# Performance work log

Hardware: AMD Instinct MI355X
Metric: run time of the kernel (lower is better)

## Reference

```python
import jax, jax.numpy as jnp
import numpy as np

N4, N3, N2, N1, K = 32768, 65536, 131072, 262144, 16
G = 512


def _w(key, fan_in, fan_out):
    return jax.random.normal(key, (fan_in, fan_out), dtype=jnp.float32) / np.sqrt(fan_in)


def setup_inputs() -> dict:
    key = jax.random.key(0)
    ks = jax.random.split(key, 24)

    def edges(k, n_coarse, n_fine):
        # each fine (output) point gathers from K random coarse (input) points
        src = jax.random.randint(k, (n_fine * K,), 0, n_coarse, dtype=jnp.int32)
        dst = jnp.repeat(jnp.arange(n_fine, dtype=jnp.int32), K)
        return src, dst

    src3, dst3 = edges(ks[0], N4, N3)
    src2, dst2 = edges(ks[1], N3, N2)
    src1, dst1 = edges(ks[2], N2, N1)

    def gidx(k, n):
        return jnp.sort(jax.random.randint(k, (n,), 0, G, dtype=jnp.int32))

    inp = {
        'z_mask': jax.random.normal(ks[3], (N4, 64), dtype=jnp.float32),
        'pos4': jax.random.normal(ks[4], (N4, 3), dtype=jnp.float32),
        'pos3': jax.random.normal(ks[5], (N3, 3), dtype=jnp.float32),
        'pos2': jax.random.normal(ks[6], (N2, 3), dtype=jnp.float32),
        'pos1': jax.random.normal(ks[7], (N1, 3), dtype=jnp.float32),
        'g4': gidx(ks[8], N4), 'g3': gidx(ks[9], N3),
        'g2': gidx(ks[10], N2), 'g1': gidx(ks[11], N1),
        # PointConv MLP params: Linear(c_in+3 -> c_mid), CELU, Linear(c_mid -> c_out), max-aggregate
        'w1a': _w(ks[12], 64 + 3, 64), 'b1a': jnp.zeros((64,), jnp.float32),
        'w1b': _w(ks[13], 64, 32), 'b1b': jnp.zeros((32,), jnp.float32),
        'w2a': _w(ks[14], 32 + 3, 16), 'b2a': jnp.zeros((16,), jnp.float32),
        'w2b': _w(ks[15], 16, 16), 'b2b': jnp.zeros((16,), jnp.float32),
        'w3a': _w(ks[16], 16 + 3, 8), 'b3a': jnp.zeros((8,), jnp.float32),
        'w3b': _w(ks[17], 8, 8), 'b3b': jnp.zeros((8,), jnp.float32),
        'wlin': _w(ks[18], 8, 1), 'blin': jnp.zeros((1,), jnp.float32),
        'src3': src3, 'dst3': dst3,
        'src2': src2, 'dst2': dst2,
        'src1': src1, 'dst1': dst1,
    }
    return inp


def point_conv(x_in, pos_in, pos_out, src, dst, w_a, b_a, w_b, b_b, n_out):
    # gather: per-edge neighbor features + relative positions
    rel = pos_in[src] - pos_out[dst]                      # [E, 3]
    feat = jnp.concatenate([x_in[src], rel], axis=-1)     # [E, c_in+3]
    h = jax.nn.celu(feat @ w_a + b_a)                     # [E, c_mid]
    m = h @ w_b + b_b                                     # [E, c_out]
    # scatter: max-aggregate edge messages onto output points
    return jax.ops.segment_max(m, dst, num_segments=n_out)


def reference(z_mask, pos4, pos3, pos2, pos1, g4, g3, g2, g1,
              w1a, b1a, w1b, b1b, w2a, b2a, w2b, b2b, w3a, b3a, w3b, b3b,
              wlin, blin, src3, dst3, src2, dst2, src1, dst1):
    out = jax.nn.celu(point_conv(z_mask, pos4, pos3, src3, dst3, w1a, b1a, w1b, b1b, N3))
    out = jax.nn.celu(point_conv(out, pos3, pos2, src2, dst2, w2a, b2a, w2b, b2b, N2))
    out = jax.nn.celu(point_conv(out, pos2, pos1, src1, dst1, w3a, b3a, w3b, b3b, N1))
    logits = out @ wlin + blin                            # [N1, 1]
    return jax.nn.log_sigmoid(logits)
```

## Files before the change

### kernel.cpp

```cpp
#include <hip/hip_runtime.h>
#include <hip/hip_fp16.h>
#include <math.h>

#define N4C 32768
#define N3C 65536
#define N2C 131072
#define N1C 262144

typedef _Float16 f16x8 __attribute__((ext_vector_type(8)));
typedef float f32x4 __attribute__((ext_vector_type(4)));
typedef float f32x16 __attribute__((ext_vector_type(16)));

__device__ __forceinline__ f32x4 mfma16(f16x8 a, f16x8 b, f32x4 c) {
  return __builtin_amdgcn_mfma_f32_16x16x32_f16(a, b, c, 0, 0, 0);
}
__device__ __forceinline__ f32x16 mfma32(f16x8 a, f16x8 b, f32x16 c) {
  return __builtin_amdgcn_mfma_f32_32x32x16_f16(a, b, c, 0, 0, 0);
}

__device__ __forceinline__ float celuf(float x) {
  return fmaxf(x, 0.f) + (__expf(fminf(x, 0.f)) - 1.f);
}

__device__ __forceinline__ float logsigf(float x) {
  float e = __expf(-fabsf(x));
  return fminf(x, 0.f) - __logf(1.f + e);
}

__device__ __forceinline__ _Float16 exp16(_Float16 x) {
  __half h; __builtin_memcpy(&h, &x, 2);
  h = hexp(h);
  _Float16 r; __builtin_memcpy(&r, &h, 2);
  return r;
}

__device__ __forceinline__ f16x8 celu8(f16x8 x) {
  f16x8 z = {};
  f16x8 mx = __builtin_elementwise_max(x, z);
  f16x8 mn = __builtin_elementwise_min(x, z);
#pragma unroll
  for (int i = 0; i < 8; ++i) mn[i] = exp16(mn[i]);
  return mx + (mn - (_Float16)1.0f);
}

__device__ __forceinline__ unsigned packh2(_Float16 a, _Float16 b) {
  union { _Float16 h[2]; unsigned u; } v; v.h[0] = a; v.h[1] = b; return v.u;
}
__device__ __forceinline__ _Float16 loh(unsigned u) {
  union { unsigned u; _Float16 h[2]; } v; v.u = u; return v.h[0];
}
__device__ __forceinline__ _Float16 hih(unsigned u) {
  union { unsigned u; _Float16 h[2]; } v; v.u = u; return v.h[1];
}

__global__ __launch_bounds__(256) void y4_kernel(
    const float* __restrict__ z, const float* __restrict__ w1a,
    const float* __restrict__ b1a, _Float16* __restrict__ y4) {
  const int lane = threadIdx.x & 63, wid = threadIdx.x >> 6;
  const int col = lane & 15, quad = lane >> 4;
  const int base = (blockIdx.x * 4 + wid) * 16;

  f16x8 Ba[2][4];
#pragma unroll
  for (int c = 0; c < 2; ++c)
#pragma unroll
    for (int t = 0; t < 4; ++t)
#pragma unroll
      for (int j = 0; j < 8; ++j)
        Ba[c][t][j] = (_Float16)w1a[(c * 32 + quad * 8 + j) * 64 + t * 16 + col];

  const float* zr = z + (size_t)(base + col) * 64;
  f16x8 A0, A1;
  {
    float4 f0 = *(const float4*)(zr + quad * 8);
    float4 f1 = *(const float4*)(zr + quad * 8 + 4);
    float4 f2 = *(const float4*)(zr + 32 + quad * 8);
    float4 f3 = *(const float4*)(zr + 32 + quad * 8 + 4);
    A0[0] = (_Float16)f0.x; A0[1] = (_Float16)f0.y; A0[2] = (_Float16)f0.z; A0[3] = (_Float16)f0.w;
    A0[4] = (_Float16)f1.x; A0[5] = (_Float16)f1.y; A0[6] = (_Float16)f1.z; A0[7] = (_Float16)f1.w;
    A1[0] = (_Float16)f2.x; A1[1] = (_Float16)f2.y; A1[2] = (_Float16)f2.z; A1[3] = (_Float16)f2.w;
    A1[4] = (_Float16)f3.x; A1[5] = (_Float16)f3.y; A1[6] = (_Float16)f3.z; A1[7] = (_Float16)f3.w;
  }
#pragma unroll
  for (int t = 0; t < 4; ++t) {
    f32x4 acc = {0.f, 0.f, 0.f, 0.f};
    acc = mfma16(A0, Ba[0][t], acc);
    acc = mfma16(A1, Ba[1][t], acc);
    const float bt = b1a[t * 16 + col];
#pragma unroll
    for (int r = 0; r < 4; ++r)
      y4[(size_t)(base + quad * 4 + r) * 64 + t * 16 + col] = (_Float16)(acc[r] + bt);
  }
}

__global__ __launch_bounds__(256) void y3_kernel(
    const _Float16* __restrict__ x3f, const float* __restrict__ w2a,
    const float* __restrict__ b2a, _Float16* __restrict__ y3) {
  const int lane = threadIdx.x & 63, wid = threadIdx.x >> 6;
  const int col = lane & 15, quad = lane >> 4;
  const int base = (blockIdx.x * 4 + wid) * 16;

  f16x8 B;
#pragma unroll
  for (int j = 0; j < 8; ++j) B[j] = (_Float16)w2a[(quad * 8 + j) * 16 + col];

  f16x8 A = *(const f16x8*)(x3f + (size_t)(base + col) * 32 + quad * 8);
  f32x4 d = {0.f, 0.f, 0.f, 0.f};
  d = mfma16(A, B, d);
  const float bt = b2a[col];
#pragma unroll
  for (int r = 0; r < 4; ++r)
    y3[(size_t)(base + quad * 4 + r) * 16 + col] = (_Float16)(d[r] + bt);
}

__global__ __launch_bounds__(256) void y2_kernel(
    const _Float16* __restrict__ x2f, const float* __restrict__ w3a,
    const float* __restrict__ b3a, _Float16* __restrict__ y2) {
  const int lane = threadIdx.x & 63, wid = threadIdx.x >> 6;
  const int col = lane & 15, quad = lane >> 4;
  const int base = (blockIdx.x * 4 + wid) * 16;

  f16x8 B;
#pragma unroll
  for (int j = 0; j < 8; ++j) {
    int k = quad * 8 + j;
    B[j] = (k < 16 && col < 8) ? (_Float16)w3a[k * 8 + col] : (_Float16)0.f;
  }
  f16x8 A = *(const f16x8*)(x2f + (size_t)(base + col) * 16 + (quad & 1) * 8);
  f32x4 d = {0.f, 0.f, 0.f, 0.f};
  d = mfma16(A, B, d);
  if (col < 8) {
    const float bt = b3a[col];
#pragma unroll
    for (int r = 0; r < 4; ++r)
      y2[(size_t)(base + quad * 4 + r) * 8 + col] = (_Float16)(d[r] + bt);
  }
}

__global__ __launch_bounds__(256) void l3_kernel(
    const _Float16* __restrict__ y4, const float* __restrict__ pos4,
    const float* __restrict__ pos3, const int* __restrict__ src3,
    const float* __restrict__ w1a, const float* __restrict__ w1b,
    const float* __restrict__ b1b, _Float16* __restrict__ x3f) {
  const int lane = threadIdx.x & 63, wid = threadIdx.x >> 6;
  const int col = lane & 15, quad = lane >> 4;

  f16x8 Bb[2][2];
#pragma unroll
  for (int c = 0; c < 2; ++c)
#pragma unroll
    for (int t = 0; t < 2; ++t)
#pragma unroll
      for (int j = 0; j < 8; ++j)
        Bb[c][t][j] = (_Float16)w1b[(c * 32 + quad * 8 + j) * 32 + t * 16 + col];
  f16x8 W0[3], W1[3];
#pragma unroll
  for (int c = 0; c < 3; ++c)
#pragma unroll
    for (int j = 0; j < 8; ++j) {
      W0[c][j] = (_Float16)w1a[(64 + c) * 64 + quad * 8 + j];
      W1[c][j] = (_Float16)w1a[(64 + c) * 64 + 32 + quad * 8 + j];
    }
  const float biasB0 = b1b[col], biasB1 = b1b[16 + col];

  const int gwave = blockIdx.x * 4 + wid;
  const int nw = gridDim.x * 4;

  for (int p = gwave; p < N3C; p += nw) {
    const int s = src3[p * 16 + col];
    const int up = __builtin_amdgcn_readfirstlane(p);
    const float po0 = pos3[up * 3 + 0];
    const float po1 = pos3[up * 3 + 1];
    const float po2 = pos3[up * 3 + 2];

    f16x8 A0 = *(const f16x8*)(y4 + (size_t)s * 64 + quad * 8);
    f16x8 A1 = *(const f16x8*)(y4 + (size_t)s * 64 + 32 + quad * 8);

    unsigned u0 = 0, u1 = 0;
    if (quad == 0) {
      _Float16 h0 = (_Float16)(pos4[s * 3 + 0] - po0);
      _Float16 h1 = (_Float16)(pos4[s * 3 + 1] - po1);
      _Float16 h2 = (_Float16)(pos4[s * 3 + 2] - po2);
      u0 = packh2(h0, h1);
      u1 = packh2(h2, (_Float16)0.f);
    }
    u0 = (unsigned)__shfl((int)u0, col, 64);
    u1 = (unsigned)__shfl((int)u1, col, 64);
    const _Float16 rr0 = loh(u0), rr1 = hih(u0), rr2 = loh(u1);

    A0 = celu8(A0 + W0[0] * rr0 + W0[1] * rr1 + W0[2] * rr2);
    A1 = celu8(A1 + W1[0] * rr0 + W1[1] * rr1 + W1[2] * rr2);

    f32x4 e[2];
#pragma unroll
    for (int t = 0; t < 2; ++t) {
      f32x4 acc = {0.f, 0.f, 0.f, 0.f};
      acc = mfma16(A0, Bb[0][t], acc);
      acc = mfma16(A1, Bb[1][t], acc);
      e[t] = acc;
    }
    float m0 = fmaxf(fmaxf(e[0][0], e[0][1]), fmaxf(e[0][2], e[0][3]));
    float m1 = fmaxf(fmaxf(e[1][0], e[1][1]), fmaxf(e[1][2], e[1][3]));
    m0 = fmaxf(m0, __shfl_xor(m0, 16, 64));
    m0 = fmaxf(m0, __shfl_xor(m0, 32, 64));
    m1 = fmaxf(m1, __shfl_xor(m1, 16, 64));
    m1 = fmaxf(m1, __shfl_xor(m1, 32, 64));
    if (lane < 16) {
      _Float16* row = x3f + (size_t)p * 32;
      row[col]      = (_Float16)celuf(m0 + biasB0);
      row[16 + col] = (_Float16)celuf(m1 + biasB1);
    }
  }
}

__global__ __launch_bounds__(256) void l2_kernel(
    const _Float16* __restrict__ y3, const float* __restrict__ pos3,
    const float* __restrict__ pos2, const int* __restrict__ src2,
    const float* __restrict__ w2a, const float* __restrict__ w2b,
    const float* __restrict__ b2b, _Float16* __restrict__ x2f) {
  const int lane = threadIdx.x & 63, wid = threadIdx.x >> 6;
  const int n = lane & 31;
  const int e = lane & 15;
  const int h = (lane >> 4) & 1;
  const int kh = lane >> 5;

  f16x8 Bb;
#pragma unroll
  for (int j = 0; j < 8; ++j)
    Bb[j] = (n < 16) ? (_Float16)w2b[(kh * 8 + j) * 16 + n] : (_Float16)0.f;
  f16x8 W[3];
#pragma unroll
  for (int c = 0; c < 3; ++c)
#pragma unroll
    for (int j = 0; j < 8; ++j)
      W[c][j] = (_Float16)w2a[(32 + c) * 16 + kh * 8 + j];
  const float biasB = b2b[n & 15];

  const int gwave = blockIdx.x * 4 + wid;
  const int nw = gridDim.x * 4;

  for (int pr = gwave; pr < N2C / 2; pr += nw) {
    const int p = 2 * pr + h;
    const int s = src2[p * 16 + e];

    f16x8 A = *(const f16x8*)(y3 + (size_t)s * 16 + kh * 8);

    unsigned u0 = 0, u1 = 0;
    if (kh == 0) {
      _Float16 h0 = (_Float16)(pos3[s * 3 + 0] - pos2[p * 3 + 0]);
      _Float16 h1 = (_Float16)(pos3[s * 3 + 1] - pos2[p * 3 + 1]);
      _Float16 h2 = (_Float16)(pos3[s * 3 + 2] - pos2[p * 3 + 2]);
      u0 = packh2(h0, h1);
      u1 = packh2(h2, (_Float16)0.f);
    }
    u0 = (unsigned)__shfl((int)u0, lane & 31, 64);
    u1 = (unsigned)__shfl((int)u1, lane & 31, 64);
    const _Float16 rr0 = loh(u0), rr1 = hih(u0), rr2 = loh(u1);

    A = celu8(A + W[0] * rr0 + W[1] * rr1 + W[2] * rr2);

    f32x16 acc = {};
    acc = mfma32(A, Bb, acc);

    float mA = acc[0], mB = acc[8];
#pragma unroll
    for (int r = 1; r < 8; ++r) {
      mA = fmaxf(mA, acc[r]);
      mB = fmaxf(mB, acc[8 + r]);
    }
    mA = fmaxf(mA, __shfl_xor(mA, 32, 64));
    mB = fmaxf(mB, __shfl_xor(mB, 32, 64));

    if (n < 16) {
      const float m = kh ? mB : mA;
      x2f[(size_t)(2 * pr + kh) * 16 + n] = (_Float16)celuf(m + biasB);
    }
  }
}

__global__ __launch_bounds__(256) void l1_kernel(
    const _Float16* __restrict__ y2, const float* __restrict__ pos2,
    const float* __restrict__ pos1, const int* __restrict__ src1,
    const float* __restrict__ w3a, const float* __restrict__ w3b,
    const float* __restrict__ b3b, const float* __restrict__ wlin,
    const float* __restrict__ blin, float* __restrict__ out) {
  const int lane = threadIdx.x & 63, wid = threadIdx.x >> 6;
  const int m = lane & 31;
  const int e = lane & 15;
  const int h = (lane >> 4) & 1;
  const int kh = lane >> 5;
  const int g = 2 * kh + h;

  f16x8 Bb;
  const int n = m;
#pragma unroll
  for (int j = 0; j < 8; ++j)
    Bb[j] = (n < 16 && (n >> 3) == kh) ? (_Float16)w3b[j * 8 + (n & 7)]
                                       : (_Float16)0.f;
  f16x8 W[3];
#pragma unroll
  for (int c = 0; c < 3; ++c)
#pragma unroll
    for (int j = 0; j < 8; ++j)
      W[c][j] = (_Float16)w3a[(16 + c) * 8 + j];
  const float biasB = (n < 16) ? b3b[n & 7] : 0.f;
  const float wl = (n < 16) ? wlin[n & 7] : 0.f;
  const float bl = blin[0];

  const int gwave = blockIdx.x * 4 + wid;
  const int nw = gridDim.x * 4;

  for (int q = gwave; q < N1C / 4; q += nw) {
    const int pb = q * 4;
    const int p = pb + g;
    const int s = src1[p * 16 + e];

    f16x8 A = *(const f16x8*)(y2 + (size_t)s * 8);
    const _Float16 rr0 = (_Float16)(pos2[s * 3 + 0] - pos1[p * 3 + 0]);
    const _Float16 rr1 = (_Float16)(pos2[s * 3 + 1] - pos1[p * 3 + 1]);
    const _Float16 rr2 = (_Float16)(pos2[s * 3 + 2] - pos1[p * 3 + 2]);
    A = celu8(A + W[0] * rr0 + W[1] * rr1 + W[2] * rr2);

    f32x16 acc = {};
    acc = mfma32(A, Bb, acc);

    float mA = acc[0], mB = acc[8];
#pragma unroll
    for (int r = 1; r < 8; ++r) {
      mA = fmaxf(mA, acc[r]);
      mB = fmaxf(mB, acc[8 + r]);
    }
    mA = fmaxf(mA, __shfl_xor(mA, 32, 64));
    mB = fmaxf(mB, __shfl_xor(mB, 32, 64));
    float tA = celuf(mA + biasB) * wl;
    float tB = celuf(mB + biasB) * wl;
    tA += __shfl_xor(tA, 1, 64);
    tA += __shfl_xor(tA, 2, 64);
    tA += __shfl_xor(tA, 4, 64);
    tB += __shfl_xor(tB, 1, 64);
    tB += __shfl_xor(tB, 2, 64);
    tB += __shfl_xor(tB, 4, 64);
    if (lane == 0) {
      float2 o; o.x = logsigf(tA + bl); o.y = logsigf(tB + bl);
      *(float2*)(out + pb) = o;
    } else if (lane == 8) {
      float2 o; o.x = logsigf(tA + bl); o.y = logsigf(tB + bl);
      *(float2*)(out + pb + 2) = o;
    }
  }
}

extern "C" void kernel_launch(void* const* d_in, const int* in_sizes, int n_in,
                              void* d_out, int out_size, void* d_ws, size_t ws_size,
                              hipStream_t stream) {
  const float* z_mask = (const float*)d_in[0];
  const float* pos4 = (const float*)d_in[1];
  const float* pos3 = (const float*)d_in[2];
  const float* pos2 = (const float*)d_in[3];
  const float* pos1 = (const float*)d_in[4];
  const float* w1a = (const float*)d_in[9];
  const float* b1a = (const float*)d_in[10];
  const float* w1b = (const float*)d_in[11];
  const float* b1b = (const float*)d_in[12];
  const float* w2a = (const float*)d_in[13];
  const float* b2a = (const float*)d_in[14];
  const float* w2b = (const float*)d_in[15];
  const float* b2b = (const float*)d_in[16];
  const float* w3a = (const float*)d_in[17];
  const float* b3a = (const float*)d_in[18];
  const float* w3b = (const float*)d_in[19];
  const float* b3b = (const float*)d_in[20];
  const float* wlin = (const float*)d_in[21];
  const float* blin = (const float*)d_in[22];
  const int* src3 = (const int*)d_in[23];
  const int* src2 = (const int*)d_in[25];
  const int* src1 = (const int*)d_in[27];

  char* w = (char*)d_ws;
  _Float16* y4  = (_Float16*)(w);
  _Float16* x3f = (_Float16*)(w + (4u << 20));
  _Float16* y3  = (_Float16*)(w + (8u << 20));
  _Float16* x2f = (_Float16*)(w + (10u << 20));
  _Float16* y2  = (_Float16*)(w + (14u << 20));
  float* out = (float*)d_out;

  y4_kernel<<<512, 256, 0, stream>>>(z_mask, w1a, b1a, y4);
  l3_kernel<<<2048, 256, 0, stream>>>(y4, pos4, pos3, src3, w1a, w1b, b1b, x3f);
  y3_kernel<<<1024, 256, 0, stream>>>(x3f, w2a, b2a, y3);
  l2_kernel<<<8192, 256, 0, stream>>>(y3, pos3, pos2, src2, w2a, w2b, b2b, x2f);
  y2_kernel<<<2048, 256, 0, stream>>>(x2f, w3a, b3a, y2);
  l1_kernel<<<8192, 256, 0, stream>>>(y2, pos2, pos1, src1, w3a, w3b, b3b,
                                      wlin, blin, out);
}
```

Before: 262.6 us.

## Fold source-position term into per-point precomputed projections to drop per-edge pos gathers

```diff
diff --git a/kernel.cpp b/kernel.cpp
--- a/kernel.cpp
+++ b/kernel.cpp
@@ -43,19 +43,10 @@
   return mx + (mn - (_Float16)1.0f);
 }
 
-__device__ __forceinline__ unsigned packh2(_Float16 a, _Float16 b) {
-  union { _Float16 h[2]; unsigned u; } v; v.h[0] = a; v.h[1] = b; return v.u;
-}
-__device__ __forceinline__ _Float16 loh(unsigned u) {
-  union { unsigned u; _Float16 h[2]; } v; v.u = u; return v.h[0];
-}
-__device__ __forceinline__ _Float16 hih(unsigned u) {
-  union { unsigned u; _Float16 h[2]; } v; v.u = u; return v.h[1];
-}
-
 __global__ __launch_bounds__(256) void y4_kernel(
-    const float* __restrict__ z, const float* __restrict__ w1a,
-    const float* __restrict__ b1a, _Float16* __restrict__ y4) {
+    const float* __restrict__ z, const float* __restrict__ pos4,
+    const float* __restrict__ w1a, const float* __restrict__ b1a,
+    _Float16* __restrict__ y4) {
   const int lane = threadIdx.x & 63, wid = threadIdx.x >> 6;
   const int col = lane & 15, quad = lane >> 4;
   const int base = (blockIdx.x * 4 + wid) * 16;
@@ -68,6 +59,22 @@
 #pragma unroll
       for (int j = 0; j < 8; ++j)
         Ba[c][t][j] = (_Float16)w1a[(c * 32 + quad * 8 + j) * 64 + t * 16 + col];
+
+  float wr[3][4];
+#pragma unroll
+  for (int c = 0; c < 3; ++c)
+#pragma unroll
+    for (int t = 0; t < 4; ++t)
+      wr[c][t] = w1a[(64 + c) * 64 + t * 16 + col];
+
+  float px[4], py[4], pz[4];
+#pragma unroll
+  for (int r = 0; r < 4; ++r) {
+    const int row = base + quad * 4 + r;
+    px[r] = pos4[row * 3 + 0];
+    py[r] = pos4[row * 3 + 1];
+    pz[r] = pos4[row * 3 + 2];
+  }
 
   const float* zr = z + (size_t)(base + col) * 64;
   f16x8 A0, A1;
@@ -88,14 +95,19 @@
     acc = mfma16(A1, Ba[1][t], acc);
     const float bt = b1a[t * 16 + col];
 #pragma unroll
-    for (int r = 0; r < 4; ++r)
-      y4[(size_t)(base + quad * 4 + r) * 64 + t * 16 + col] = (_Float16)(acc[r] + bt);
+    for (int r = 0; r < 4; ++r) {
+      const float posterm =
+          px[r] * wr[0][t] + py[r] * wr[1][t] + pz[r] * wr[2][t];
+      y4[(size_t)(base + quad * 4 + r) * 64 + t * 16 + col] =
+          (_Float16)(acc[r] + bt + posterm);
+    }
   }
 }
 
 __global__ __launch_bounds__(256) void y3_kernel(
-    const _Float16* __restrict__ x3f, const float* __restrict__ w2a,
-    const float* __restrict__ b2a, _Float16* __restrict__ y3) {
+    const _Float16* __restrict__ x3f, const float* __restrict__ pos3,
+    const float* __restrict__ w2a, const float* __restrict__ b2a,
+    _Float16* __restrict__ y3) {
   const int lane = threadIdx.x & 63, wid = threadIdx.x >> 6;
   const int col = lane & 15, quad = lane >> 4;
   const int base = (blockIdx.x * 4 + wid) * 16;
@@ -103,19 +115,36 @@
   f16x8 B;
 #pragma unroll
   for (int j = 0; j < 8; ++j) B[j] = (_Float16)w2a[(quad * 8 + j) * 16 + col];
+
+  float wr[3];
+#pragma unroll
+  for (int c = 0; c < 3; ++c) wr[c] = w2a[(32 + c) * 16 + col];
+
+  float px[4], py[4], pz[4];
+#pragma unroll
+  for (int r = 0; r < 4; ++r) {
+    const int row = base + quad * 4 + r;
+    px[r] = pos3[row * 3 + 0];
+    py[r] = pos3[row * 3 + 1];
+    pz[r] = pos3[row * 3 + 2];
+  }
 
   f16x8 A = *(const f16x8*)(x3f + (size_t)(base + col) * 32 + quad * 8);
   f32x4 d = {0.f, 0.f, 0.f, 0.f};
   d = mfma16(A, B, d);
   const float bt = b2a[col];
 #pragma unroll
-  for (int r = 0; r < 4; ++r)
-    y3[(size_t)(base + quad * 4 + r) * 16 + col] = (_Float16)(d[r] + bt);
+  for (int r = 0; r < 4; ++r) {
+    const float posterm = px[r] * wr[0] + py[r] * wr[1] + pz[r] * wr[2];
+    y3[(size_t)(base + quad * 4 + r) * 16 + col] =
+        (_Float16)(d[r] + bt + posterm);
+  }
 }
 
 __global__ __launch_bounds__(256) void y2_kernel(
-    const _Float16* __restrict__ x2f, const float* __restrict__ w3a,
-    const float* __restrict__ b3a, _Float16* __restrict__ y2) {
+    const _Float16* __restrict__ x2f, const float* __restrict__ pos2,
+    const float* __restrict__ w3a, const float* __restrict__ b3a,
+    _Float16* __restrict__ y2) {
   const int lane = threadIdx.x & 63, wid = threadIdx.x >> 6;
   const int col = lane & 15, quad = lane >> 4;
   const int base = (blockIdx.x * 4 + wid) * 16;
@@ -130,18 +159,26 @@
   f32x4 d = {0.f, 0.f, 0.f, 0.f};
   d = mfma16(A, B, d);
   if (col < 8) {
+    float wr[3];
+#pragma unroll
+    for (int c = 0; c < 3; ++c) wr[c] = w3a[(16 + c) * 8 + col];
     const float bt = b3a[col];
 #pragma unroll
-    for (int r = 0; r < 4; ++r)
-      y2[(size_t)(base + quad * 4 + r) * 8 + col] = (_Float16)(d[r] + bt);
+    for (int r = 0; r < 4; ++r) {
+      const int row = base + quad * 4 + r;
+      const float posterm = pos2[row * 3 + 0] * wr[0] +
+                            pos2[row * 3 + 1] * wr[1] +
+                            pos2[row * 3 + 2] * wr[2];
+      y2[(size_t)row * 8 + col] = (_Float16)(d[r] + bt + posterm);
+    }
   }
 }
 
 __global__ __launch_bounds__(256) void l3_kernel(
-    const _Float16* __restrict__ y4, const float* __restrict__ pos4,
-    const float* __restrict__ pos3, const int* __restrict__ src3,
-    const float* __restrict__ w1a, const float* __restrict__ w1b,
-    const float* __restrict__ b1b, _Float16* __restrict__ x3f) {
+    const _Float16* __restrict__ y4, const float* __restrict__ pos3,
+    const int* __restrict__ src3, const float* __restrict__ w1a,
+    const float* __restrict__ w1b, const float* __restrict__ b1b,
+    _Float16* __restrict__ x3f) {
   const int lane = threadIdx.x & 63, wid = threadIdx.x >> 6;
   const int col = lane & 15, quad = lane >> 4;
 
@@ -169,27 +206,18 @@
   for (int p = gwave; p < N3C; p += nw) {
     const int s = src3[p * 16 + col];
     const int up = __builtin_amdgcn_readfirstlane(p);
-    const float po0 = pos3[up * 3 + 0];
-    const float po1 = pos3[up * 3 + 1];
-    const float po2 = pos3[up * 3 + 2];
+    const _Float16 q0 = (_Float16)pos3[up * 3 + 0];
+    const _Float16 q1 = (_Float16)pos3[up * 3 + 1];
+    const _Float16 q2 = (_Float16)pos3[up * 3 + 2];
 
     f16x8 A0 = *(const f16x8*)(y4 + (size_t)s * 64 + quad * 8);
     f16x8 A1 = *(const f16x8*)(y4 + (size_t)s * 64 + 32 + quad * 8);
 
-    unsigned u0 = 0, u1 = 0;
-    if (quad == 0) {
-      _Float16 h0 = (_Float16)(pos4[s * 3 + 0] - po0);
-      _Float16 h1 = (_Float16)(pos4[s * 3 + 1] - po1);
-      _Float16 h2 = (_Float16)(pos4[s * 3 + 2] - po2);
-      u0 = packh2(h0, h1);
-      u1 = packh2(h2, (_Float16)0.f);
-    }
-    u0 = (unsigned)__shfl((int)u0, col, 64);
-    u1 = (unsigned)__shfl((int)u1, col, 64);
-    const _Float16 rr0 = loh(u0), rr1 = hih(u0), rr2 = loh(u1);
-
-    A0 = celu8(A0 + W0[0] * rr0 + W0[1] * rr1 + W0[2] * rr2);
-    A1 = celu8(A1 + W1[0] * rr0 + W1[1] * rr1 + W1[2] * rr2);
+    const f16x8 v0 = W0[0] * q0 + W0[1] * q1 + W0[2] * q2;
+    const f16x8 v1 = W1[0] * q0 + W1[1] * q1 + W1[2] * q2;
+
+    A0 = celu8(A0 - v0);
+    A1 = celu8(A1 - v1);
 
     f32x4 e[2];
 #pragma unroll
@@ -214,10 +242,10 @@
 }
 
 __global__ __launch_bounds__(256) void l2_kernel(
-    const _Float16* __restrict__ y3, const float* __restrict__ pos3,
-    const float* __restrict__ pos2, const int* __restrict__ src2,
-    const float* __restrict__ w2a, const float* __restrict__ w2b,
-    const float* __restrict__ b2b, _Float16* __restrict__ x2f) {
+    const _Float16* __restrict__ y3, const float* __restrict__ pos2,
+    const int* __restrict__ src2, const float* __restrict__ w2a,
+    const float* __restrict__ w2b, const float* __restrict__ b2b,
+    _Float16* __restrict__ x2f) {
   const int lane = threadIdx.x & 63, wid = threadIdx.x >> 6;
   const int n = lane & 31;
   const int e = lane & 15;
@@ -243,21 +271,13 @@
     const int p = 2 * pr + h;
     const int s = src2[p * 16 + e];
 
+    const _Float16 q0 = (_Float16)pos2[p * 3 + 0];
+    const _Float16 q1 = (_Float16)pos2[p * 3 + 1];
+    const _Float16 q2 = (_Float16)pos2[p * 3 + 2];
+
     f16x8 A = *(const f16x8*)(y3 + (size_t)s * 16 + kh * 8);
-
-    unsigned u0 = 0, u1 = 0;
-    if (kh == 0) {
-      _Float16 h0 = (_Float16)(pos3[s * 3 + 0] - pos2[p * 3 + 0]);
-      _Float16 h1 = (_Float16)(pos3[s * 3 + 1] - pos2[p * 3 + 1]);
-      _Float16 h2 = (_Float16)(pos3[s * 3 + 2] - pos2[p * 3 + 2]);
-      u0 = packh2(h0, h1);
-      u1 = packh2(h2, (_Float16)0.f);
-    }
-    u0 = (unsigned)__shfl((int)u0, lane & 31, 64);
-    u1 = (unsigned)__shfl((int)u1, lane & 31, 64);
-    const _Float16 rr0 = loh(u0), rr1 = hih(u0), rr2 = loh(u1);
-
-    A = celu8(A + W[0] * rr0 + W[1] * rr1 + W[2] * rr2);
+    const f16x8 v = W[0] * q0 + W[1] * q1 + W[2] * q2;
+    A = celu8(A - v);
 
     f32x16 acc = {};
     acc = mfma32(A, Bb, acc);
@@ -279,11 +299,11 @@
 }
 
 __global__ __launch_bounds__(256) void l1_kernel(
-    const _Float16* __restrict__ y2, const float* __restrict__ pos2,
-    const float* __restrict__ pos1, const int* __restrict__ src1,
-    const float* __restrict__ w3a, const float* __restrict__ w3b,
-    const float* __restrict__ b3b, const float* __restrict__ wlin,
-    const float* __restrict__ blin, float* __restrict__ out) {
+    const _Float16* __restrict__ y2, const float* __restrict__ pos1,
+    const int* __restrict__ src1, const float* __restrict__ w3a,
+    const float* __restrict__ w3b, const float* __restrict__ b3b,
+    const float* __restrict__ wlin, const float* __restrict__ blin,
+    float* __restrict__ out) {
   const int lane = threadIdx.x & 63, wid = threadIdx.x >> 6;
   const int m = lane & 31;
   const int e = lane & 15;
@@ -315,11 +335,13 @@
     const int p = pb + g;
     const int s = src1[p * 16 + e];
 
+    const _Float16 q0 = (_Float16)pos1[p * 3 + 0];
+    const _Float16 q1 = (_Float16)pos1[p * 3 + 1];
+    const _Float16 q2 = (_Float16)pos1[p * 3 + 2];
+
     f16x8 A = *(const f16x8*)(y2 + (size_t)s * 8);
-    const _Float16 rr0 = (_Float16)(pos2[s * 3 + 0] - pos1[p * 3 + 0]);
-    const _Float16 rr1 = (_Float16)(pos2[s * 3 + 1] - pos1[p * 3 + 1]);
-    const _Float16 rr2 = (_Float16)(pos2[s * 3 + 2] - pos1[p * 3 + 2]);
-    A = celu8(A + W[0] * rr0 + W[1] * rr1 + W[2] * rr2);
+    const f16x8 v = W[0] * q0 + W[1] * q1 + W[2] * q2;
+    A = celu8(A - v);
 
     f32x16 acc = {};
     acc = mfma32(A, Bb, acc);
@@ -384,11 +406,11 @@
   _Float16* y2  = (_Float16*)(w + (14u << 20));
   float* out = (float*)d_out;
 
-  y4_kernel<<<512, 256, 0, stream>>>(z_mask, w1a, b1a, y4);
-  l3_kernel<<<2048, 256, 0, stream>>>(y4, pos4, pos3, src3, w1a, w1b, b1b, x3f);
-  y3_kernel<<<1024, 256, 0, stream>>>(x3f, w2a, b2a, y3);
-  l2_kernel<<<8192, 256, 0, stream>>>(y3, pos3, pos2, src2, w2a, w2b, b2b, x2f);
-  y2_kernel<<<2048, 256, 0, stream>>>(x2f, w3a, b3a, y2);
-  l1_kernel<<<8192, 256, 0, stream>>>(y2, pos2, pos1, src1, w3a, w3b, b3b,
+  y4_kernel<<<512, 256, 0, stream>>>(z_mask, pos4, w1a, b1a, y4);
+  l3_kernel<<<2048, 256, 0, stream>>>(y4, pos3, src3, w1a, w1b, b1b, x3f);
+  y3_kernel<<<1024, 256, 0, stream>>>(x3f, pos3, w2a, b2a, y3);
+  l2_kernel<<<8192, 256, 0, stream>>>(y3, pos2, src2, w2a, w2b, b2b, x2f);
+  y2_kernel<<<2048, 256, 0, stream>>>(x2f, pos2, w3a, b3a, y2);
+  l1_kernel<<<8192, 256, 0, stream>>>(y2, pos1, src1, w3a, w3b, b3b,
                                       wlin, blin, out);
 }
```

New measurement: 251.9 us. 4.1% less time.
